# Kernel optimization log

Measured on AMD Instinct MI355X. Metric: run time of the kernel, lower is better.

## Reference

```python
import jax, jax.numpy as jnp
import numpy as np

N_COM = 40000
N_POS = 40000
E = 1000000
D = 128


def setup_inputs() -> dict:
    key = jax.random.key(0)
    ks = jax.random.split(key, 20)
    def idx(k, n):
        return jax.random.randint(k, (E,), 0, n)
    inp = {
        "com_emb": jax.random.normal(ks[0], (N_COM, D), jnp.float32),
        "pos_emb": jax.random.normal(ks[1], (N_POS, D), jnp.float32),
        # Demand: company -> position
        "demand_src": idx(ks[2], N_COM), "demand_dst": idx(ks[3], N_POS),
        "demand_w": jax.random.uniform(ks[4], (E,), jnp.float32),
        # Supply: position -> company
        "supply_src": idx(ks[5], N_POS), "supply_dst": idx(ks[6], N_COM),
        "supply_w": jax.random.uniform(ks[7], (E,), jnp.float32),
        # CompanyFlow: company -> company
        "cflow_src": idx(ks[8], N_COM), "cflow_dst": idx(ks[9], N_COM),
        "cflow_w": jax.random.uniform(ks[10], (E,), jnp.float32),
        # PositionFlow: position -> position
        "pflow_src": idx(ks[11], N_POS), "pflow_dst": idx(ks[12], N_POS),
        "pflow_w": jax.random.uniform(ks[13], (E,), jnp.float32),
    }
    s = float(1.0 / np.sqrt(D))
    for i, name in enumerate(["demand", "supply", "cflow", "pflow"]):
        inp[f"W_{name}"] = jax.random.uniform(ks[14 + i], (D, D), jnp.float32, -s, s)
        inp[f"b_{name}"] = jnp.zeros((D,), jnp.float32)
    return inp


def _graph_conv(h_src, src, dst, w, W, b, n_src, n_dst):
    # dgl EdgeWeightNorm(norm='both') on the relation subgraph:
    # w_norm = w / sqrt(weighted_out_deg(src) * weighted_in_deg(dst))
    deg_out = jax.ops.segment_sum(w, src, num_segments=n_src)  # [n_src]
    deg_in = jax.ops.segment_sum(w, dst, num_segments=n_dst)   # [n_dst]
    wn = w * jax.lax.rsqrt(deg_out[src] * deg_in[dst])         # [E]
    # dgl GraphConv(norm='none'): project first (in==out feats), then
    # weighted gather/scatter-sum aggregation, bias, ReLU activation.
    msg = (h_src @ W)[src] * wn[:, None]                       # [E, D]
    agg = jax.ops.segment_sum(msg, dst, num_segments=n_dst)    # [n_dst, D]
    return jax.nn.relu(agg + b)


def reference(com_emb, pos_emb,
              demand_src, demand_dst, demand_w,
              supply_src, supply_dst, supply_w,
              cflow_src, cflow_dst, cflow_w,
              pflow_src, pflow_dst, pflow_w,
              W_demand, b_demand, W_supply, b_supply,
              W_cflow, b_cflow, W_pflow, b_pflow):
    demand = _graph_conv(com_emb, demand_src, demand_dst, demand_w, W_demand, b_demand, N_COM, N_POS)
    pflow = _graph_conv(pos_emb, pflow_src, pflow_dst, pflow_w, W_pflow, b_pflow, N_POS, N_POS)
    supply = _graph_conv(pos_emb, supply_src, supply_dst, supply_w, W_supply, b_supply, N_POS, N_COM)
    cflow = _graph_conv(com_emb, cflow_src, cflow_dst, cflow_w, W_cflow, b_cflow, N_COM, N_COM)
    # HeteroGraphConv aggregate='mean' over relations per destination ntype
    com_out = 0.5 * (supply + cflow)   # [N_COM, D]
    pos_out = 0.5 * (demand + pflow)   # [N_POS, D]
    return jnp.stack([com_out, pos_out])  # [2, N, D] (stacked ntype dict)
```

## Files before the change

kernel.cpp:

```cpp
#include <hip/hip_runtime.h>
#include <hip/hip_fp16.h>

#define D   128
#define NN  40000
#define NB  625
#define GH  64
#define GF  128

typedef unsigned long long ull;
typedef __attribute__((ext_vector_type(8))) _Float16 f16x8;
typedef __attribute__((ext_vector_type(4))) float f32x4;

struct Ptrs { const int* src[4]; const int* dst[4]; const float* w[4]; };

__global__ __launch_bounds__(256) void conv_kernel(
    const float* __restrict__ in, __half* __restrict__ out, int n8)
{
    int i = blockIdx.x * 256 + threadIdx.x;
    if (i >= n8) return;
    const float4* a = (const float4*)in + (size_t)i * 2;
    float4 v0 = a[0], v1 = a[1];
    __half2 pack[4];
    pack[0] = __floats2half2_rn(v0.x, v0.y);
    pack[1] = __floats2half2_rn(v0.z, v0.w);
    pack[2] = __floats2half2_rn(v1.x, v1.y);
    pack[3] = __floats2half2_rn(v1.z, v1.w);
    ((float4*)out)[i] = *(float4*)pack;
}

__global__ __launch_bounds__(256) void wpack_kernel(
    const float* __restrict__ W0, const float* __restrict__ W1,
    const float* __restrict__ W2, const float* __restrict__ W3,
    __half* __restrict__ wp)
{
    int t = blockIdx.x * 256 + threadIdx.x;
    int rel = t >> 11;
    int idx = t & 2047;
    int lane = idx & 63;
    int ct = (idx >> 6) & 7;
    int kt = idx >> 9;
    const float* W = rel == 0 ? W0 : rel == 1 ? W1 : rel == 2 ? W2 : W3;
    int k0 = kt * 32 + (lane >> 4) * 8;
    int col = ct * 16 + (lane & 15);
    __half tmp[8];
#pragma unroll
    for (int j = 0; j < 8; ++j)
        tmp[j] = __float2half_rn(W[(size_t)(k0 + j) * D + col]);
    *(float4*)(wp + (size_t)t * 8) = *(float4*)tmp;
}

__global__ __launch_bounds__(1024) void hist_kernel(
    Ptrs p, __half* __restrict__ histo16, int E)
{
    __shared__ float hist[NN];
    const int bx  = blockIdx.x;
    const int rel = bx >> 6;
    const int rep = bx & (GH - 1);
    const int tid = threadIdx.x;

    for (int i = tid; i < NN; i += 1024) hist[i] = 0.f;
    __syncthreads();

    const int es  = (E + GH - 1) / GH;
    const int beg = rep * es;
    const int end = min(beg + es, E);
    const int* idx = p.src[rel];
    const float* w = p.w[rel];
    for (int e = beg + tid; e < end; e += 1024)
        atomicAdd(&hist[idx[e]], w[e]);
    __syncthreads();

    __half2* outp = (__half2*)(histo16 + (size_t)bx * NN);
    for (int i = tid; i < NN / 2; i += 1024)
        outp[i] = __floats2half2_rn(hist[2 * i], hist[2 * i + 1]);
}

__global__ __launch_bounds__(256) void reduce_kernel(
    const __half* __restrict__ histo16, float* __restrict__ rdego, int total)
{
    int i = blockIdx.x * 256 + threadIdx.x;
    if (i >= total) return;
    int rel = i / NN;
    int node = i - rel * NN;
    const __half* bp = histo16 + (size_t)rel * GH * NN + node;
    float v = 0.f;
#pragma unroll
    for (int r = 0; r < GH; ++r) v += __half2float(bp[(size_t)r * NN]);
    rdego[i] = rsqrtf(v);
}

__global__ __launch_bounds__(256) void bcnt_kernel(
    Ptrs p, int* __restrict__ cnt_store, int E)
{
    __shared__ int cnt[NB];
    const int rel = blockIdx.x / GF;
    const int rep = blockIdx.x - rel * GF;
    const int tid = threadIdx.x;
    for (int b = tid; b < NB; b += 256) cnt[b] = 0;
    __syncthreads();
    const int es  = (E + GF - 1) / GF;
    const int beg = rep * es;
    const int end = min(beg + es, E);
    const int* dst = p.dst[rel];
    for (int e = beg + tid; e < end; e += 256)
        atomicAdd(&cnt[dst[e] >> 6], 1);
    __syncthreads();
    for (int b = tid; b < NB; b += 256)
        cnt_store[((size_t)(rel * NB + b)) * GF + rep] = cnt[b];
}

__device__ inline int block_excl_scan(int v, int tid) {
    __shared__ int wsum[16];
    int lane = tid & 63, wid = tid >> 6;
    int x = v;
#pragma unroll
    for (int off = 1; off < 64; off <<= 1) {
        int y = __shfl_up(x, off, 64);
        if (lane >= off) x += y;
    }
    if (lane == 63) wsum[wid] = x;
    __syncthreads();
    if (wid == 0) {
        int y = (lane < 16) ? wsum[lane] : 0;
#pragma unroll
        for (int off = 1; off < 16; off <<= 1) {
            int t = __shfl_up(y, off, 64);
            if (lane >= off) y += t;
        }
        if (lane < 16) wsum[lane] = y;
    }
    __syncthreads();
    int woff = wid ? wsum[wid - 1] : 0;
    return woff + x - v;
}

__global__ __launch_bounds__(1024) void scan1_kernel(
    const int* __restrict__ cnt_store, int* __restrict__ scanex,
    int* __restrict__ bsum, int total)
{
    int tid = threadIdx.x;
    int i = blockIdx.x * 1024 + tid;
    int v = (i < total) ? cnt_store[i] : 0;
    int excl = block_excl_scan(v, tid);
    if (i < total) scanex[i] = excl;
    if (tid == 1023) bsum[blockIdx.x] = excl + v;
}

__global__ __launch_bounds__(1024) void scan2_kernel(int* __restrict__ bsum, int nb)
{
    int tid = threadIdx.x;
    int v = (tid < nb) ? bsum[tid] : 0;
    int excl = block_excl_scan(v, tid);
    if (tid < nb) bsum[tid] = excl;
}

__global__ __launch_bounds__(256) void scan3_kernel(
    const int* __restrict__ scanex, const int* __restrict__ bsum,
    int* __restrict__ cursor_base, int* __restrict__ bucket_ptr,
    int total, int E)
{
    int i = blockIdx.x * 256 + threadIdx.x;
    if (i >= total) return;
    int v = scanex[i] + bsum[i >> 10];
    int rel = i / (NB * GF);
    int rem = i - rel * (NB * GF);
    int b = rem / GF, rep = rem - b * GF;
    int local = v - rel * E;
    cursor_base[i] = local;
    if (rep == 0) bucket_ptr[rel * (NB + 1) + b] = local;
    if (rem == 0) bucket_ptr[rel * (NB + 1) + NB] = E;
}

__global__ __launch_bounds__(512) void fill4_kernel(
    Ptrs p, const int* __restrict__ cursor_base,
    ull* __restrict__ csr8, int E)
{
    __shared__ int lcur[NB];
    const int rel = blockIdx.x / GF;
    const int rep = blockIdx.x - rel * GF;
    const int tid = threadIdx.x;
    const int* cb = cursor_base + (size_t)rel * NB * GF;
    for (int b = tid; b < NB; b += 512)
        lcur[b] = cb[(size_t)b * GF + rep];
    __syncthreads();
    const int es  = (E + GF - 1) / GF;
    const int beg = rep * es;
    const int end = min(beg + es, E);
    const int* src = p.src[rel];
    const int* dst = p.dst[rel];
    const float* w = p.w[rel];
    ull* c8 = csr8 + (size_t)rel * E;
    for (int e = beg + tid; e < end; e += 512) {
        int s = src[e];
        int d = dst[e];
        int pos = atomicAdd(&lcur[d >> 6], 1);
        ull rec = (ull)(unsigned)(s | ((d & 63) << 16)) |
                  ((ull)__float_as_uint(w[e]) << 32);
        c8[pos] = rec;
    }
}

__global__ __launch_bounds__(256) void sort24_kernel(
    const int* __restrict__ bucket_ptr, const ull* __restrict__ csr8,
    const float* __restrict__ rdego, unsigned* __restrict__ csr2u,
    int* __restrict__ row_ptr, int E)
{
    __shared__ int cnt[64];
    __shared__ int cur[64];
    __shared__ float swsum[64];
    const int rel = blockIdx.x / NB;
    const int b   = blockIdx.x - rel * NB;
    const int tid = threadIdx.x;
    const int* bp_r = bucket_ptr + rel * (NB + 1);
    const ull* c8 = csr8 + (size_t)rel * E;
    unsigned* c2 = csr2u + (size_t)rel * E;
    int* rp_r = row_ptr + rel * (NN + 1);
    const float* rd = rdego + (size_t)rel * NN;
    const int beg = bp_r[b];
    const int end = bp_r[b + 1];
    if (tid < 64) { cnt[tid] = 0; swsum[tid] = 0.f; }
    __syncthreads();
    for (int e = beg + tid; e < end; e += 256) {
        ull rec = c8[e];
        int j = (int)((rec >> 16) & 63);
        atomicAdd(&cnt[j], 1);
        atomicAdd(&swsum[j], __uint_as_float((unsigned)(rec >> 32)));
    }
    __syncthreads();
    if (tid < 64) {
        int v = cnt[tid];
        int x = v;
#pragma unroll
        for (int off = 1; off < 64; off <<= 1) {
            int y = __shfl_up(x, off, 64);
            if (tid >= off) x += y;
        }
        int start = beg + x - v;
        cur[tid] = start;
        rp_r[b * 64 + tid] = start;
        swsum[tid] = rsqrtf(swsum[tid]);
        if (b == 0 && tid == 0) rp_r[NN] = E;
    }
    __syncthreads();
    for (int e = beg + tid; e < end; e += 256) {
        ull rec = c8[e];
        int j = (int)((rec >> 16) & 63);
        int s = (int)(rec & 0xFFFF);
        float wn = __uint_as_float((unsigned)(rec >> 32)) * rd[s] * swsum[j];
        int pos = atomicAdd(&cur[j], 1);
        c2[pos] = (unsigned)s |
                  ((unsigned)__half_as_ushort(__float2half_rn(wn)) << 16);
    }
}

__global__ __launch_bounds__(256) void gather4_kernel(
    const int* __restrict__ row_ptr, const unsigned* __restrict__ csr2u,
    const __half* __restrict__ h16com, const __half* __restrict__ h16pos,
    __half* __restrict__ agg16, int gBlocks, int E)
{
    int rel = blockIdx.x / gBlocks;
    int lb  = blockIdx.x - rel * gBlocks;
    int node = (lb * 256 + threadIdx.x) >> 6;
    int lane = threadIdx.x & 63;
    if (node >= NN) return;
    const int* rp = row_ptr + rel * (NN + 1);
    const unsigned* c2 = csr2u + (size_t)rel * E;
    const __half* h16 = (rel == 0 || rel == 3) ? h16com : h16pos;
    __half* agg = agg16 + (size_t)rel * NN * D;

    int beg = rp[node], end = rp[node + 1];
    const int g = lane >> 4, l16 = lane & 15;

    float acc[8] = {};
    for (int e = beg; e < end; e += 4) {
        int ee = e + g;
        int valid = ee < end;
        unsigned rec = __builtin_nontemporal_load(c2 + (valid ? ee : (end - 1)));
        int s = (int)(rec & 0xFFFF);
        float wn = valid ? __half2float(__ushort_as_half((unsigned short)(rec >> 16))) : 0.f;
        f32x4 hv4 = ((const f32x4*)(h16 + (size_t)s * D))[l16];
        __half2* hp = (__half2*)&hv4;
        float2 f0 = __half22float2(hp[0]);
        float2 f1 = __half22float2(hp[1]);
        float2 f2 = __half22float2(hp[2]);
        float2 f3 = __half22float2(hp[3]);
        acc[0] += wn * f0.x; acc[1] += wn * f0.y;
        acc[2] += wn * f1.x; acc[3] += wn * f1.y;
        acc[4] += wn * f2.x; acc[5] += wn * f2.y;
        acc[6] += wn * f3.x; acc[7] += wn * f3.y;
    }
#pragma unroll
    for (int k = 0; k < 8; ++k) {
        acc[k] += __shfl_xor(acc[k], 16, 64);
        acc[k] += __shfl_xor(acc[k], 32, 64);
    }
    if (g == 0) {
        __half2 pack[4];
        pack[0] = __floats2half2_rn(acc[0], acc[1]);
        pack[1] = __floats2half2_rn(acc[2], acc[3]);
        pack[2] = __floats2half2_rn(acc[4], acc[5]);
        pack[3] = __floats2half2_rn(acc[6], acc[7]);
        __builtin_nontemporal_store(*(f32x4*)pack,
                                    (f32x4*)(agg + (size_t)node * D) + l16);
    }
}

__global__ __launch_bounds__(256) void projmf_kernel(
    const __half* __restrict__ aggA, const __half* __restrict__ wpA,
    const float* __restrict__ bA,
    const __half* __restrict__ aggB, const __half* __restrict__ wpB,
    const float* __restrict__ bB, float* __restrict__ outh)
{
    __shared__ char As[2][64 * 256];
    const int t = threadIdx.x;
    const int row0 = blockIdx.x * 64;

    for (int r2 = 0; r2 < 2; ++r2) {
        const float4* src = (const float4*)((r2 ? aggB : aggA) + (size_t)row0 * D);
        for (int i = t; i < 1024; i += 256) {
            int row = i >> 4, ch = i & 15;
            int byte = row * 256 + ch * 16;
            byte ^= (row & 7) << 4;
            *(float4*)(As[r2] + byte) = src[i];
        }
    }
    __syncthreads();

    const int wv = t >> 6, lane = t & 63;
    const int rbase = wv * 16;

    f16x8 aA[4], aB[4];
#pragma unroll
    for (int kt = 0; kt < 4; ++kt) {
        int row = rbase + (lane & 15);
        int byte = row * 256 + kt * 64 + (lane >> 4) * 16;
        byte ^= (row & 7) << 4;
        aA[kt] = *(const f16x8*)(As[0] + byte);
        aB[kt] = *(const f16x8*)(As[1] + byte);
    }

    f32x4 accA[8], accB[8];
#pragma unroll
    for (int i = 0; i < 8; ++i) {
        accA[i] = (f32x4){0.f, 0.f, 0.f, 0.f};
        accB[i] = (f32x4){0.f, 0.f, 0.f, 0.f};
    }

#pragma unroll
    for (int ct = 0; ct < 8; ++ct) {
#pragma unroll
        for (int kt = 0; kt < 4; ++kt) {
            f16x8 bfA = *(const f16x8*)(wpA + ((size_t)((kt * 8 + ct) * 64 + lane)) * 8);
            f16x8 bfB = *(const f16x8*)(wpB + ((size_t)((kt * 8 + ct) * 64 + lane)) * 8);
            accA[ct] = __builtin_amdgcn_mfma_f32_16x16x32_f16(aA[kt], bfA, accA[ct], 0, 0, 0);
            accB[ct] = __builtin_amdgcn_mfma_f32_16x16x32_f16(aB[kt], bfB, accB[ct], 0, 0, 0);
        }
    }

#pragma unroll
    for (int ct = 0; ct < 8; ++ct) {
        int col = ct * 16 + (lane & 15);
        float ba = bA[col], bb = bB[col];
#pragma unroll
        for (int v = 0; v < 4; ++v) {
            int row = row0 + rbase + (lane >> 4) * 4 + v;
            float r = 0.5f * (fmaxf(accA[ct][v] + ba, 0.f) +
                              fmaxf(accB[ct][v] + bb, 0.f));
            outh[(size_t)row * D + col] = r;
        }
    }
}

extern "C" void kernel_launch(void* const* d_in, const int* in_sizes, int n_in,
                              void* d_out, int out_size, void* d_ws, size_t ws_size,
                              hipStream_t stream) {
    const float* com_emb = (const float*)d_in[0];
    const float* pos_emb = (const float*)d_in[1];
    const int E = in_sizes[2];
    const int N = NN;

    float* out = (float*)d_out;
    float* out_com = out;
    float* out_pos = out + (size_t)N * D;

    Ptrs ptrs;
    ptrs.src[0] = (const int*)d_in[8];  ptrs.dst[0] = (const int*)d_in[9];  ptrs.w[0] = (const float*)d_in[10];
    ptrs.src[1] = (const int*)d_in[5];  ptrs.dst[1] = (const int*)d_in[6];  ptrs.w[1] = (const float*)d_in[7];
    ptrs.src[2] = (const int*)d_in[11]; ptrs.dst[2] = (const int*)d_in[12]; ptrs.w[2] = (const float*)d_in[13];
    ptrs.src[3] = (const int*)d_in[2];  ptrs.dst[3] = (const int*)d_in[3];  ptrs.w[3] = (const float*)d_in[4];

    const int totalCnt = 4 * NB * GF;
    char* p = (char*)d_ws;
    float* rdego       = (float*)p;  p += (size_t)4 * N * 4;
    int*   cnt_store   = (int*)p;    p += (size_t)totalCnt * 4;
    int*   scanex      = (int*)p;    p += (size_t)totalCnt * 4;
    int*   bsum        = (int*)p;    p += (size_t)1024 * 4;
    int*   cursor_base = (int*)p;    p += (size_t)totalCnt * 4;
    int*   bucket_ptr  = (int*)p;    p += (size_t)4 * (NB + 1) * 4;
    int*   row_ptr     = (int*)p;    p += (size_t)4 * (N + 1) * 4;
    ull*   csr8        = (ull*)p;    p += (size_t)4 * E * 8;
    unsigned* csr2u    = (unsigned*)p; p += (size_t)4 * E * 4;
    __half* h16com     = (__half*)p; p += (size_t)N * D * 2;
    __half* h16pos     = (__half*)p; p += (size_t)N * D * 2;
    __half* agg16      = (__half*)p; p += (size_t)4 * N * D * 2;
    __half* wpack      = (__half*)p; p += (size_t)4 * 2048 * 8 * 2;
    __half* histo16    = (__half*)p;

    const int cBlocks = (N * D / 8 + 255) / 256;
    const int gBlocks = N / 4;
    const int sBlocks = (totalCnt + 1023) / 1024;

    conv_kernel<<<cBlocks, 256, 0, stream>>>(com_emb, h16com, N * D / 8);
    conv_kernel<<<cBlocks, 256, 0, stream>>>(pos_emb, h16pos, N * D / 8);
    wpack_kernel<<<32, 256, 0, stream>>>((const float*)d_in[18], (const float*)d_in[16],
                                         (const float*)d_in[20], (const float*)d_in[14],
                                         wpack);

    hist_kernel<<<4 * GH, 1024, 0, stream>>>(ptrs, histo16, E);
    reduce_kernel<<<(4 * N + 255) / 256, 256, 0, stream>>>(histo16, rdego, 4 * N);
    bcnt_kernel<<<4 * GF, 256, 0, stream>>>(ptrs, cnt_store, E);
    scan1_kernel<<<sBlocks, 1024, 0, stream>>>(cnt_store, scanex, bsum, totalCnt);
    scan2_kernel<<<1, 1024, 0, stream>>>(bsum, sBlocks);
    scan3_kernel<<<(totalCnt + 255) / 256, 256, 0, stream>>>(scanex, bsum, cursor_base,
                                                             bucket_ptr, totalCnt, E);

    fill4_kernel<<<4 * GF, 512, 0, stream>>>(ptrs, cursor_base, csr8, E);
    sort24_kernel<<<4 * NB, 256, 0, stream>>>(bucket_ptr, csr8, rdego, csr2u, row_ptr, E);
    gather4_kernel<<<4 * gBlocks, 256, 0, stream>>>(row_ptr, csr2u, h16com, h16pos,
                                                    agg16, gBlocks, E);

    projmf_kernel<<<N / 64, 256, 0, stream>>>(
        agg16 + (size_t)1 * N * D, wpack + (size_t)1 * 16384, (const float*)d_in[17],
        agg16 + (size_t)0 * N * D, wpack + (size_t)0 * 16384, (const float*)d_in[19],
        out_com);
    projmf_kernel<<<N / 64, 256, 0, stream>>>(
        agg16 + (size_t)3 * N * D, wpack + (size_t)3 * 16384, (const float*)d_in[15],
        agg16 + (size_t)2 * N * D, wpack + (size_t)2 * 16384, (const float*)d_in[21],
        out_pos);
}
```

Measured before the change: 355.1 us.

## Partition gather by source-node quarter for cache locality and fuse bucket counting

Each destination row's edges are sub-sorted into four source-node ranges, so the gather runs one source quarter at a time, with block ordering grouped by quarter, to keep the gathered feature rows resident in L2. Each quarter writes its own partial aggregate buffer, which a new reduction kernel sums in half precision. Bucket counting is folded into the histogram kernel, removing a separate pass over the dst arrays, and the fill split drops from 128 to 64 partitions. The cost is four times the aggregate memory, an extra reduction pass and extra fp16 rounding of partial sums. The histogram scratch now aliases the aggregate buffer.

```diff
diff --git a/kernel.cpp b/kernel.cpp
--- a/kernel.cpp
+++ b/kernel.cpp
@@ -3,9 +3,9 @@
 
 #define D   128
 #define NN  40000
+#define NQ  10000
 #define NB  625
-#define GH  64
-#define GF  128
+#define GS  64
 
 typedef unsigned long long ull;
 typedef __attribute__((ext_vector_type(8))) _Float16 f16x8;
@@ -50,29 +50,36 @@
 }
 
 __global__ __launch_bounds__(1024) void hist_kernel(
-    Ptrs p, __half* __restrict__ histo16, int E)
+    Ptrs p, __half* __restrict__ histo16, int* __restrict__ cnt_store, int E)
 {
     __shared__ float hist[NN];
+    __shared__ int cnt[NB];
     const int bx  = blockIdx.x;
     const int rel = bx >> 6;
-    const int rep = bx & (GH - 1);
+    const int rep = bx & (GS - 1);
     const int tid = threadIdx.x;
 
     for (int i = tid; i < NN; i += 1024) hist[i] = 0.f;
-    __syncthreads();
-
-    const int es  = (E + GH - 1) / GH;
+    for (int i = tid; i < NB; i += 1024) cnt[i] = 0;
+    __syncthreads();
+
+    const int es  = (E + GS - 1) / GS;
     const int beg = rep * es;
     const int end = min(beg + es, E);
-    const int* idx = p.src[rel];
+    const int* srcp = p.src[rel];
+    const int* dstp = p.dst[rel];
     const float* w = p.w[rel];
-    for (int e = beg + tid; e < end; e += 1024)
-        atomicAdd(&hist[idx[e]], w[e]);
+    for (int e = beg + tid; e < end; e += 1024) {
+        atomicAdd(&hist[srcp[e]], w[e]);
+        atomicAdd(&cnt[dstp[e] >> 6], 1);
+    }
     __syncthreads();
 
     __half2* outp = (__half2*)(histo16 + (size_t)bx * NN);
     for (int i = tid; i < NN / 2; i += 1024)
         outp[i] = __floats2half2_rn(hist[2 * i], hist[2 * i + 1]);
+    for (int b = tid; b < NB; b += 1024)
+        cnt_store[((size_t)(rel * NB + b)) * GS + rep] = cnt[b];
 }
 
 __global__ __launch_bounds__(256) void reduce_kernel(
@@ -82,31 +89,11 @@
     if (i >= total) return;
     int rel = i / NN;
     int node = i - rel * NN;
-    const __half* bp = histo16 + (size_t)rel * GH * NN + node;
+    const __half* bp = histo16 + (size_t)rel * GS * NN + node;
     float v = 0.f;
 #pragma unroll
-    for (int r = 0; r < GH; ++r) v += __half2float(bp[(size_t)r * NN]);
+    for (int r = 0; r < GS; ++r) v += __half2float(bp[(size_t)r * NN]);
     rdego[i] = rsqrtf(v);
-}
-
-__global__ __launch_bounds__(256) void bcnt_kernel(
-    Ptrs p, int* __restrict__ cnt_store, int E)
-{
-    __shared__ int cnt[NB];
-    const int rel = blockIdx.x / GF;
-    const int rep = blockIdx.x - rel * GF;
-    const int tid = threadIdx.x;
-    for (int b = tid; b < NB; b += 256) cnt[b] = 0;
-    __syncthreads();
-    const int es  = (E + GF - 1) / GF;
-    const int beg = rep * es;
-    const int end = min(beg + es, E);
-    const int* dst = p.dst[rel];
-    for (int e = beg + tid; e < end; e += 256)
-        atomicAdd(&cnt[dst[e] >> 6], 1);
-    __syncthreads();
-    for (int b = tid; b < NB; b += 256)
-        cnt_store[((size_t)(rel * NB + b)) * GF + rep] = cnt[b];
 }
 
 __device__ inline int block_excl_scan(int v, int tid) {
@@ -162,9 +149,9 @@
     int i = blockIdx.x * 256 + threadIdx.x;
     if (i >= total) return;
     int v = scanex[i] + bsum[i >> 10];
-    int rel = i / (NB * GF);
-    int rem = i - rel * (NB * GF);
-    int b = rem / GF, rep = rem - b * GF;
+    int rel = i / (NB * GS);
+    int rem = i - rel * (NB * GS);
+    int b = rem / GS, rep = rem - b * GS;
     int local = v - rel * E;
     cursor_base[i] = local;
     if (rep == 0) bucket_ptr[rel * (NB + 1) + b] = local;
@@ -176,14 +163,14 @@
     ull* __restrict__ csr8, int E)
 {
     __shared__ int lcur[NB];
-    const int rel = blockIdx.x / GF;
-    const int rep = blockIdx.x - rel * GF;
+    const int rel = blockIdx.x / GS;
+    const int rep = blockIdx.x - rel * GS;
     const int tid = threadIdx.x;
-    const int* cb = cursor_base + (size_t)rel * NB * GF;
+    const int* cb = cursor_base + (size_t)rel * NB * GS;
     for (int b = tid; b < NB; b += 512)
-        lcur[b] = cb[(size_t)b * GF + rep];
-    __syncthreads();
-    const int es  = (E + GF - 1) / GF;
+        lcur[b] = cb[(size_t)b * GS + rep];
+    __syncthreads();
+    const int es  = (E + GS - 1) / GS;
     const int beg = rep * es;
     const int end = min(beg + es, E);
     const int* src = p.src[rel];
@@ -200,13 +187,13 @@
     }
 }
 
-__global__ __launch_bounds__(256) void sort24_kernel(
+__global__ __launch_bounds__(256) void sort24q_kernel(
     const int* __restrict__ bucket_ptr, const ull* __restrict__ csr8,
     const float* __restrict__ rdego, unsigned* __restrict__ csr2u,
-    int* __restrict__ row_ptr, int E)
-{
-    __shared__ int cnt[64];
-    __shared__ int cur[64];
+    int* __restrict__ rpq, int E)
+{
+    __shared__ int cnt[256];
+    __shared__ int cur[256];
     __shared__ float swsum[64];
     const int rel = blockIdx.x / NB;
     const int b   = blockIdx.x - rel * NB;
@@ -214,61 +201,63 @@
     const int* bp_r = bucket_ptr + rel * (NB + 1);
     const ull* c8 = csr8 + (size_t)rel * E;
     unsigned* c2 = csr2u + (size_t)rel * E;
-    int* rp_r = row_ptr + rel * (NN + 1);
+    int* rpq_r = rpq + (size_t)rel * (4 * NN + 1);
     const float* rd = rdego + (size_t)rel * NN;
     const int beg = bp_r[b];
     const int end = bp_r[b + 1];
-    if (tid < 64) { cnt[tid] = 0; swsum[tid] = 0.f; }
+    cnt[tid] = 0;
+    if (tid < 64) swsum[tid] = 0.f;
     __syncthreads();
     for (int e = beg + tid; e < end; e += 256) {
         ull rec = c8[e];
-        int j = (int)((rec >> 16) & 63);
-        atomicAdd(&cnt[j], 1);
-        atomicAdd(&swsum[j], __uint_as_float((unsigned)(rec >> 32)));
-    }
-    __syncthreads();
-    if (tid < 64) {
+        int dl = (int)((rec >> 16) & 63);
+        int s  = (int)(rec & 0xFFFF);
+        atomicAdd(&cnt[dl * 4 + s / NQ], 1);
+        atomicAdd(&swsum[dl], __uint_as_float((unsigned)(rec >> 32)));
+    }
+    __syncthreads();
+    {
         int v = cnt[tid];
-        int x = v;
-#pragma unroll
-        for (int off = 1; off < 64; off <<= 1) {
-            int y = __shfl_up(x, off, 64);
-            if (tid >= off) x += y;
-        }
-        int start = beg + x - v;
+        int excl = block_excl_scan(v, tid);
+        int start = beg + excl;
         cur[tid] = start;
-        rp_r[b * 64 + tid] = start;
-        swsum[tid] = rsqrtf(swsum[tid]);
-        if (b == 0 && tid == 0) rp_r[NN] = E;
-    }
+        rpq_r[b * 256 + tid] = start;
+        if (b == 0 && tid == 0) rpq_r[4 * NN] = E;
+    }
+    if (tid < 64) swsum[tid] = rsqrtf(swsum[tid]);
     __syncthreads();
     for (int e = beg + tid; e < end; e += 256) {
         ull rec = c8[e];
-        int j = (int)((rec >> 16) & 63);
-        int s = (int)(rec & 0xFFFF);
-        float wn = __uint_as_float((unsigned)(rec >> 32)) * rd[s] * swsum[j];
-        int pos = atomicAdd(&cur[j], 1);
+        int dl = (int)((rec >> 16) & 63);
+        int s  = (int)(rec & 0xFFFF);
+        float wn = __uint_as_float((unsigned)(rec >> 32)) * rd[s] * swsum[dl];
+        int pos = atomicAdd(&cur[dl * 4 + s / NQ], 1);
         c2[pos] = (unsigned)s |
                   ((unsigned)__half_as_ushort(__float2half_rn(wn)) << 16);
     }
 }
 
-__global__ __launch_bounds__(256) void gather4_kernel(
-    const int* __restrict__ row_ptr, const unsigned* __restrict__ csr2u,
+__global__ __launch_bounds__(256) void gather4q_kernel(
+    const int* __restrict__ rpq, const unsigned* __restrict__ csr2u,
     const __half* __restrict__ h16com, const __half* __restrict__ h16pos,
-    __half* __restrict__ agg16, int gBlocks, int E)
-{
-    int rel = blockIdx.x / gBlocks;
-    int lb  = blockIdx.x - rel * gBlocks;
-    int node = (lb * 256 + threadIdx.x) >> 6;
+    __half* __restrict__ aggQ, int E)
+{
+    int i = blockIdx.x;
+    int x = i & 7;
+    int q = x >> 1;
+    int t = (i >> 3) * 2 + (x & 1);
+    int rel = t / (NN / 4);
+    int nb  = t - rel * (NN / 4);
+    int wv   = threadIdx.x >> 6;
     int lane = threadIdx.x & 63;
-    if (node >= NN) return;
-    const int* rp = row_ptr + rel * (NN + 1);
+    int node = nb * 4 + wv;
+
+    const int* rp = rpq + (size_t)rel * (4 * NN + 1);
     const unsigned* c2 = csr2u + (size_t)rel * E;
     const __half* h16 = (rel == 0 || rel == 3) ? h16com : h16pos;
-    __half* agg = agg16 + (size_t)rel * NN * D;
-
-    int beg = rp[node], end = rp[node + 1];
+    __half* agg = aggQ + ((size_t)q * 4 + rel) * NN * D;
+
+    int beg = rp[node * 4 + q], end = rp[node * 4 + q + 1];
     const int g = lane >> 4, l16 = lane & 15;
 
     float acc[8] = {};
@@ -305,6 +294,32 @@
     }
 }
 
+__global__ __launch_bounds__(256) void reduceAgg_kernel(
+    __half* __restrict__ aggQ, int n4)
+{
+    int i = blockIdx.x * 256 + threadIdx.x;
+    if (i >= n4) return;
+    const size_t stride = (size_t)n4;
+    float4* base = (float4*)aggQ;
+    float out[8] = {};
+#pragma unroll
+    for (int q = 0; q < 4; ++q) {
+        float4 v = base[i + stride * q];
+        __half2* hp = (__half2*)&v;
+#pragma unroll
+        for (int k = 0; k < 4; ++k) {
+            float2 f = __half22float2(hp[k]);
+            out[2 * k]     += f.x;
+            out[2 * k + 1] += f.y;
+        }
+    }
+    __half2 pack[4];
+#pragma unroll
+    for (int k = 0; k < 4; ++k)
+        pack[k] = __floats2half2_rn(out[2 * k], out[2 * k + 1]);
+    base[i] = *(float4*)pack;
+}
+
 __global__ __launch_bounds__(256) void projmf_kernel(
     const __half* __restrict__ aggA, const __half* __restrict__ wpA,
     const float* __restrict__ bA,
@@ -389,7 +404,7 @@
     ptrs.src[2] = (const int*)d_in[11]; ptrs.dst[2] = (const int*)d_in[12]; ptrs.w[2] = (const float*)d_in[13];
     ptrs.src[3] = (const int*)d_in[2];  ptrs.dst[3] = (const int*)d_in[3];  ptrs.w[3] = (const float*)d_in[4];
 
-    const int totalCnt = 4 * NB * GF;
+    const int totalCnt = 4 * NB * GS;
     char* p = (char*)d_ws;
     float* rdego       = (float*)p;  p += (size_t)4 * N * 4;
     int*   cnt_store   = (int*)p;    p += (size_t)totalCnt * 4;
@@ -397,17 +412,16 @@
     int*   bsum        = (int*)p;    p += (size_t)1024 * 4;
     int*   cursor_base = (int*)p;    p += (size_t)totalCnt * 4;
     int*   bucket_ptr  = (int*)p;    p += (size_t)4 * (NB + 1) * 4;
-    int*   row_ptr     = (int*)p;    p += (size_t)4 * (N + 1) * 4;
+    int*   rpq         = (int*)p;    p += (size_t)4 * (4 * N + 1) * 4;
     ull*   csr8        = (ull*)p;    p += (size_t)4 * E * 8;
     unsigned* csr2u    = (unsigned*)p; p += (size_t)4 * E * 4;
     __half* h16com     = (__half*)p; p += (size_t)N * D * 2;
     __half* h16pos     = (__half*)p; p += (size_t)N * D * 2;
-    __half* agg16      = (__half*)p; p += (size_t)4 * N * D * 2;
     __half* wpack      = (__half*)p; p += (size_t)4 * 2048 * 8 * 2;
-    __half* histo16    = (__half*)p;
+    __half* aggQ       = (__half*)p;
+    __half* histo16    = aggQ;
 
     const int cBlocks = (N * D / 8 + 255) / 256;
-    const int gBlocks = N / 4;
     const int sBlocks = (totalCnt + 1023) / 1024;
 
     conv_kernel<<<cBlocks, 256, 0, stream>>>(com_emb, h16com, N * D / 8);
@@ -416,25 +430,27 @@
                                          (const float*)d_in[20], (const float*)d_in[14],
                                          wpack);
 
-    hist_kernel<<<4 * GH, 1024, 0, stream>>>(ptrs, histo16, E);
+    hist_kernel<<<4 * GS, 1024, 0, stream>>>(ptrs, histo16, cnt_store, E);
     reduce_kernel<<<(4 * N + 255) / 256, 256, 0, stream>>>(histo16, rdego, 4 * N);
-    bcnt_kernel<<<4 * GF, 256, 0, stream>>>(ptrs, cnt_store, E);
     scan1_kernel<<<sBlocks, 1024, 0, stream>>>(cnt_store, scanex, bsum, totalCnt);
     scan2_kernel<<<1, 1024, 0, stream>>>(bsum, sBlocks);
     scan3_kernel<<<(totalCnt + 255) / 256, 256, 0, stream>>>(scanex, bsum, cursor_base,
                                                              bucket_ptr, totalCnt, E);
 
-    fill4_kernel<<<4 * GF, 512, 0, stream>>>(ptrs, cursor_base, csr8, E);
-    sort24_kernel<<<4 * NB, 256, 0, stream>>>(bucket_ptr, csr8, rdego, csr2u, row_ptr, E);
-    gather4_kernel<<<4 * gBlocks, 256, 0, stream>>>(row_ptr, csr2u, h16com, h16pos,
-                                                    agg16, gBlocks, E);
+    fill4_kernel<<<4 * GS, 512, 0, stream>>>(ptrs, cursor_base, csr8, E);
+    sort24q_kernel<<<4 * NB, 256, 0, stream>>>(bucket_ptr, csr8, rdego, csr2u, rpq, E);
+
+    gather4q_kernel<<<16 * (N / 4) * 4 / 4, 256, 0, stream>>>(rpq, csr2u, h16com, h16pos,
+                                                              aggQ, E);
+    const int n4 = 4 * N * D / 8;
+    reduceAgg_kernel<<<(n4 + 255) / 256, 256, 0, stream>>>(aggQ, n4);
 
     projmf_kernel<<<N / 64, 256, 0, stream>>>(
-        agg16 + (size_t)1 * N * D, wpack + (size_t)1 * 16384, (const float*)d_in[17],
-        agg16 + (size_t)0 * N * D, wpack + (size_t)0 * 16384, (const float*)d_in[19],
+        aggQ + (size_t)1 * N * D, wpack + (size_t)1 * 16384, (const float*)d_in[17],
+        aggQ + (size_t)0 * N * D, wpack + (size_t)0 * 16384, (const float*)d_in[19],
         out_com);
     projmf_kernel<<<N / 64, 256, 0, stream>>>(
-        agg16 + (size_t)3 * N * D, wpack + (size_t)3 * 16384, (const float*)d_in[15],
-        agg16 + (size_t)2 * N * D, wpack + (size_t)2 * 16384, (const float*)d_in[21],
+        aggQ + (size_t)3 * N * D, wpack + (size_t)3 * 16384, (const float*)d_in[15],
+        aggQ + (size_t)2 * N * D, wpack + (size_t)2 * 16384, (const float*)d_in[21],
         out_pos);
 }
```

Result: slower. 469.6 us (+32.2%).
